# Kernel optimization log

Measured on AMD Instinct MI355X. Metric: run time of the kernel, lower is better.

## Reference

```python
import jax, jax.numpy as jnp
import numpy as np

B, S, D = 2, 2048, 2048
H, HD = 16, 128
P = 2048  # past (cached) kv length


def setup_inputs() -> dict:
    key = jax.random.key(0)
    ks = jax.random.split(key, 12)
    sw = 1.0 / np.sqrt(D)
    inp = {
        "x": jax.random.normal(ks[0], (B, S, D), jnp.float32),
        "past_k": jax.random.normal(ks[1], (B, H, P, HD), jnp.float32),
        "past_v": jax.random.normal(ks[2], (B, H, P, HD), jnp.float32),
        "Wq": jax.random.normal(ks[3], (D, D), jnp.float32) * sw,
        "bq": jax.random.normal(ks[4], (D,), jnp.float32) * 0.01,
        "Wk": jax.random.normal(ks[5], (D, D), jnp.float32) * sw,
        "bk": jax.random.normal(ks[6], (D,), jnp.float32) * 0.01,
        "Wv": jax.random.normal(ks[7], (D, D), jnp.float32) * sw,
        "bv": jax.random.normal(ks[8], (D,), jnp.float32) * 0.01,
        "Wo": jax.random.normal(ks[9], (D, D), jnp.float32) * sw,
        "bo": jax.random.normal(ks[10], (D,), jnp.float32) * 0.01,
    }
    return inp


def _heads(t):
    # [B, S, D] -> [B, H, S, HD]
    return t.reshape(B, -1, H, HD).transpose(0, 2, 1, 3)


def reference(x, past_k, past_v, Wq, bq, Wk, bk, Wv, bv, Wo, bo):
    # QKV projections (separate weights, _qkv_same_embed_dim=False path)
    q = _heads(x @ Wq.T + bq)          # [B,H,S,HD]
    k_new = _heads(x @ Wk.T + bk)      # [B,H,S,HD]
    v_new = _heads(x @ Wv.T + bv)

    # KV cache append
    k_cached = jnp.concatenate([past_k, k_new], axis=2)  # [B,H,P+S,HD]
    v_cached = jnp.concatenate([past_v, v_new], axis=2)
    cached_len = P + S

    # Manual attention path (query_seq_len != cached_seq_len)
    scale = 1.0 / np.sqrt(HD)
    scores = jnp.einsum('bhqd,bhkd->bhqk', q, k_cached) * scale  # [B,H,S,P+S]
    q_pos = jnp.arange(cached_len - S, cached_len)[:, None]
    k_pos = jnp.arange(cached_len)[None, :]
    mask = q_pos >= k_pos  # offset causal mask [S, P+S]
    scores = jnp.where(mask, scores, -jnp.inf)
    attn = jax.nn.softmax(scores, axis=-1)
    out = jnp.einsum('bhqk,bhkd->bhqd', attn, v_cached)  # [B,H,S,HD]

    out = out.transpose(0, 2, 1, 3).reshape(B, S, D)
    return out @ Wo.T + bo
```

## Files before the change

### kernel.cpp

```cpp
#include <hip/hip_runtime.h>

typedef unsigned short u16;
typedef __attribute__((ext_vector_type(4))) float f32x4;
typedef __attribute__((ext_vector_type(8))) short s16x8;

#define CEXP 0.12751742929f

static __device__ __forceinline__ u16 f2bf(float x) {
  unsigned u = __float_as_uint(x);
  u = u + 0x7fffu + ((u >> 16) & 1u);
  return (u16)(u >> 16);
}
static __device__ __forceinline__ unsigned pack2bf(float a, float b) {
  return (unsigned)f2bf(a) | ((unsigned)f2bf(b) << 16);
}
static __device__ __forceinline__ f32x4 fzero() { f32x4 z; z[0]=0.f; z[1]=0.f; z[2]=0.f; z[3]=0.f; return z; }
static __device__ __forceinline__ f32x4 mfma16(s16x8 a, s16x8 b, f32x4 c) {
  return __builtin_amdgcn_mfma_f32_16x16x32_bf16(a, b, c, 0, 0, 0);
}
static __device__ __forceinline__ void gld16(const void* g, void* l) {
  __builtin_amdgcn_global_load_lds((const __attribute__((address_space(1))) void*)g,
                                   (__attribute__((address_space(3))) void*)l, 16, 0, 0);
}

__global__ void cvt_kernel(const float* __restrict__ s, u16* __restrict__ d, int n4, int lg) {
  int stride = gridDim.x * blockDim.x;
  for (int i4 = blockIdx.x * blockDim.x + threadIdx.x; i4 < n4; i4 += stride) {
    int i = i4 * 4;
    float4 v = *reinterpret_cast<const float4*>(s + i);
    size_t di = (size_t)i + ((size_t)(i >> lg) << lg);
    ushort4 o;
    o.x = f2bf(v.x); o.y = f2bf(v.y); o.z = f2bf(v.z); o.w = f2bf(v.w);
    *reinterpret_cast<ushort4*>(d + di) = o;
  }
}

__global__ void transpose_past_v(const float* __restrict__ src, u16* __restrict__ dst) {
  __shared__ u16 tile[64 * 138];
  int bh = blockIdx.y, pt = blockIdx.x;
  const float* s = src + ((size_t)bh * 2048 + (size_t)pt * 64) * 128;
  int t = threadIdx.x;
#pragma unroll
  for (int it = 0; it < 8; ++it) {
    int idx = it * 1024 + t * 4;
    int row = idx >> 7, col = idx & 127;
    float4 v = *reinterpret_cast<const float4*>(s + idx);
    u16* d = &tile[row * 138 + col];
    d[0] = f2bf(v.x); d[1] = f2bf(v.y); d[2] = f2bf(v.z); d[3] = f2bf(v.w);
  }
  __syncthreads();
  size_t dbase = (size_t)bh * 128 * 4096 + (size_t)pt * 64;
#pragma unroll
  for (int it = 0; it < 32; ++it) {
    int o = it * 256 + t;
    int dd = o >> 6, pos = o & 63;
    dst[dbase + (size_t)dd * 4096 + pos] = tile[pos * 138 + dd];
  }
}

__global__ void transpose_new_v(const u16* __restrict__ src, u16* __restrict__ dst) {
  __shared__ u16 tile[64 * 138];
  int bh = blockIdx.y, pt = blockIdx.x;
  const u16* s = src + ((size_t)bh * 2048 + (size_t)pt * 64) * 128;
  int t = threadIdx.x;
#pragma unroll
  for (int it = 0; it < 8; ++it) {
    int idx = it * 1024 + t * 4;
    int row = idx >> 7, col = idx & 127;
    ushort4 v = *reinterpret_cast<const ushort4*>(s + idx);
    u16* d = &tile[row * 138 + col];
    d[0] = v.x; d[1] = v.y; d[2] = v.z; d[3] = v.w;
  }
  __syncthreads();
  size_t dbase = (size_t)bh * 128 * 4096 + 2048 + (size_t)pt * 64;
#pragma unroll
  for (int it = 0; it < 32; ++it) {
    int o = it * 256 + t;
    int dd = o >> 6, pos = o & 63;
    dst[dbase + (size_t)dd * 4096 + pos] = tile[pos * 138 + dd];
  }
}

static __device__ __forceinline__ void gemm_core(const u16* __restrict__ A, const u16* __restrict__ Wn,
                                                 int m0, char* ldsb, f32x4 (&acc)[4][4]) {
  const int tid = threadIdx.x;
  const int w = tid >> 6, lane = tid & 63, g = lane >> 4, ln = lane & 15;
#pragma unroll
  for (int mi = 0; mi < 4; ++mi)
#pragma unroll
    for (int ni = 0; ni < 4; ++ni) acc[mi][ni] = fzero();

  auto stage = [&](int buf, int k0) {
#pragma unroll
    for (int i = 0; i < 2; ++i) {
      int c = w * 2 + i;
      int p = c * 1024 + lane * 16;
      int row = p >> 6;
      int colb = (p & 63) ^ ((row & 3) << 4);
      const u16* sa = A + (size_t)(m0 + row) * 2048 + k0 + (colb >> 1);
      const u16* sw = Wn + (size_t)row * 2048 + k0 + (colb >> 1);
      char* da = ldsb + buf * 16384 + c * 1024;
      gld16(sa, da);
      gld16(sw, da + 8192);
    }
  };
  stage(0, 0);
  __syncthreads();
  const int wr = w >> 1, wc = w & 1;
  for (int kt = 0; kt < 64; ++kt) {
    int cur = kt & 1;
    if (kt < 63) stage(cur ^ 1, (kt + 1) * 32);
    const char* bp = ldsb + cur * 16384;
    s16x8 af[4], bw[4];
#pragma unroll
    for (int mi = 0; mi < 4; ++mi) {
      int row = wr * 64 + mi * 16 + ln;
      int lin = row * 64 + g * 16;
      af[mi] = *reinterpret_cast<const s16x8*>(bp + (lin ^ ((row & 3) << 4)));
    }
#pragma unroll
    for (int ni = 0; ni < 4; ++ni) {
      int row = wc * 64 + ni * 16 + ln;
      int lin = row * 64 + g * 16;
      bw[ni] = *reinterpret_cast<const s16x8*>(bp + 8192 + (lin ^ ((row & 3) << 4)));
    }
#pragma unroll
    for (int mi = 0; mi < 4; ++mi)
#pragma unroll
      for (int ni = 0; ni < 4; ++ni)
        acc[mi][ni] = mfma16(af[mi], bw[ni], acc[mi][ni]);
    __syncthreads();
  }
}

__global__ __launch_bounds__(256, 3) void qkv_gemm(const u16* __restrict__ xb,
    const u16* __restrict__ wq, const u16* __restrict__ wk, const u16* __restrict__ wv,
    const float* __restrict__ bq, const float* __restrict__ bk, const float* __restrict__ bv,
    u16* __restrict__ outq, u16* __restrict__ kc, u16* __restrict__ outv) {
  __shared__ char ldsb[32768];
  int m0 = blockIdx.x * 128;
  int ny = blockIdx.y;
  int wsel = ny >> 4, n0 = (ny & 15) * 128;
  const u16* W; const float* bias; u16* dst; int lrow, off;
  if (wsel == 0)      { W = wq; bias = bq; dst = outq; lrow = 2048; off = 0; }
  else if (wsel == 1) { W = wk; bias = bk; dst = kc;   lrow = 4096; off = 2048; }
  else                { W = wv; bias = bv; dst = outv; lrow = 2048; off = 0; }
  f32x4 acc[4][4];
  gemm_core(xb, W + (size_t)n0 * 2048, m0, ldsb, acc);
  const int tid = threadIdx.x, w = tid >> 6, lane = tid & 63, g = lane >> 4, ln = lane & 15;
  const int wr = w >> 1, wc = w & 1;
#pragma unroll
  for (int ni = 0; ni < 4; ++ni) {
    int j = n0 + wc * 64 + ni * 16 + ln;
    float bcol = bias[j];
    int h = j >> 7, hd = j & 127;
#pragma unroll
    for (int mi = 0; mi < 4; ++mi) {
#pragma unroll
      for (int r = 0; r < 4; ++r) {
        int rowg = m0 + wr * 64 + mi * 16 + g * 4 + r;
        int b = rowg >> 11, s = rowg & 2047;
        float val = acc[mi][ni][r] + bcol;
        dst[((size_t)(b * 16 + h) * lrow + off + s) * 128 + hd] = f2bf(val);
      }
    }
  }
}

__global__ __launch_bounds__(256, 3) void proj_gemm(const u16* __restrict__ ao, const u16* __restrict__ wo,
    const float* __restrict__ bo, float* __restrict__ out) {
  __shared__ char ldsb[32768];
  int m0 = blockIdx.x * 128, n0 = blockIdx.y * 128;
  f32x4 acc[4][4];
  gemm_core(ao, wo + (size_t)n0 * 2048, m0, ldsb, acc);
  const int tid = threadIdx.x, w = tid >> 6, lane = tid & 63, g = lane >> 4, ln = lane & 15;
  const int wr = w >> 1, wc = w & 1;
#pragma unroll
  for (int ni = 0; ni < 4; ++ni) {
    int j = n0 + wc * 64 + ni * 16 + ln;
    float bcol = bo[j];
#pragma unroll
    for (int mi = 0; mi < 4; ++mi) {
#pragma unroll
      for (int r = 0; r < 4; ++r) {
        int rowg = m0 + wr * 64 + mi * 16 + g * 4 + r;
        out[(size_t)rowg * 2048 + j] = acc[mi][ni][r] + bcol;
      }
    }
  }
}

__global__ __launch_bounds__(256, 2) void attn_kernel(const u16* __restrict__ Qb,
    const u16* __restrict__ Kc, const u16* __restrict__ Vt, u16* __restrict__ Ao) {
  __shared__ char lds[65536];
  const int tid = threadIdx.x, w = tid >> 6, lane = tid & 63, g = lane >> 4, ln = lane & 15;
  const int bh = blockIdx.y, qbk = blockIdx.x;
  const int b = bh >> 4, h = bh & 15;
  const u16* Qbh = Qb + (size_t)bh * 2048 * 128;
  const u16* Kbh = Kc + (size_t)bh * 4096 * 128;
  const u16* Vbh = Vt + (size_t)bh * 128 * 4096;

  const int qrow0 = qbk * 128 + w * 32;
  s16x8 qf[2][4];
#pragma unroll
  for (int nt = 0; nt < 2; ++nt)
#pragma unroll
    for (int ks = 0; ks < 4; ++ks)
      qf[nt][ks] = *reinterpret_cast<const s16x8*>(Qbh + (size_t)(qrow0 + nt * 16 + ln) * 128 + ks * 32 + g * 8);

  f32x4 o[2][8];
#pragma unroll
  for (int qt = 0; qt < 2; ++qt)
#pragma unroll
    for (int nd = 0; nd < 8; ++nd) o[qt][nd] = fzero();
  float mrun[2] = {-3e38f, -3e38f}, lrun[2] = {0.f, 0.f};

  const int qpmin = 2048 + qrow0;
  const int ntiles = (2048 + qbk * 128 + 128) >> 6;

  auto stage = [&](int buf, int kv0) {
    char* base = lds + buf * 32768;
#pragma unroll
    for (int i = 0; i < 4; ++i) {
      int p = (w * 4 + i) * 1024 + lane * 16;
      int row = p >> 8;
      int colb = (p & 255) ^ ((row & 7) << 4);
      gld16(Kbh + (size_t)(kv0 + row) * 128 + (colb >> 1), base + (w * 4 + i) * 1024);
      int vrow = p >> 7;
      int vcol = (p & 127) ^ ((vrow & 7) << 4);
      gld16(Vbh + (size_t)vrow * 4096 + kv0 + (vcol >> 1), base + 16384 + (w * 4 + i) * 1024);
    }
  };

  stage(0, 0);
  __syncthreads();
  for (int t = 0; t < ntiles; ++t) {
    int cur = t & 1;
    int kv0 = t * 64;
    if (t + 1 < ntiles) stage(cur ^ 1, kv0 + 64);
    const char* Kl = lds + cur * 32768;
    const char* Vl = Kl + 16384;
    bool active = kv0 <= qpmin + 31;
    if (active) {
      f32x4 sf[4][2];
#pragma unroll
      for (int mt = 0; mt < 4; ++mt) { sf[mt][0] = fzero(); sf[mt][1] = fzero(); }
#pragma unroll
      for (int ks = 0; ks < 4; ++ks) {
#pragma unroll
        for (int mt = 0; mt < 4; ++mt) {
          int row = mt * 16 + ln;
          int lin = row * 256 + ks * 64 + g * 16;
          s16x8 a = *reinterpret_cast<const s16x8*>(Kl + (lin ^ ((row & 7) << 4)));
          sf[mt][0] = mfma16(a, qf[0][ks], sf[mt][0]);
          sf[mt][1] = mfma16(a, qf[1][ks], sf[mt][1]);
        }
      }
      if (kv0 + 63 > qpmin) {
#pragma unroll
        for (int mt = 0; mt < 4; ++mt)
#pragma unroll
          for (int nt = 0; nt < 2; ++nt)
#pragma unroll
            for (int r = 0; r < 4; ++r) {
              int kvg = kv0 + mt * 16 + g * 4 + r;
              int qp = 2048 + qrow0 + nt * 16 + ln;
              if (kvg > qp) sf[mt][nt][r] = -3e38f;
            }
      }
      float fac[2];
#pragma unroll
      for (int nt = 0; nt < 2; ++nt) {
        float pm = sf[0][nt][0];
#pragma unroll
        for (int mt = 0; mt < 4; ++mt)
#pragma unroll
          for (int r = 0; r < 4; ++r) pm = fmaxf(pm, sf[mt][nt][r]);
        pm = fmaxf(pm, __shfl_xor(pm, 16));
        pm = fmaxf(pm, __shfl_xor(pm, 32));
        float mnew = (pm > mrun[nt] + 8.f) ? pm : mrun[nt];
        float f = exp2f((mrun[nt] - mnew) * CEXP);
        mrun[nt] = mnew; fac[nt] = f;
        float rs = 0.f;
#pragma unroll
        for (int mt = 0; mt < 4; ++mt)
#pragma unroll
          for (int r = 0; r < 4; ++r) {
            float p = exp2f((sf[mt][nt][r] - mnew) * CEXP);
            sf[mt][nt][r] = p; rs += p;
          }
        rs += __shfl_xor(rs, 16); rs += __shfl_xor(rs, 32);
        lrun[nt] = lrun[nt] * f + rs;
      }
      if (!__all((fac[0] == 1.f) & (fac[1] == 1.f))) {
#pragma unroll
        for (int qt = 0; qt < 2; ++qt) {
          float fr[4];
#pragma unroll
          for (int r = 0; r < 4; ++r) fr[r] = __shfl(fac[qt], g * 4 + r);
#pragma unroll
          for (int nd = 0; nd < 8; ++nd) {
            o[qt][nd][0] *= fr[0]; o[qt][nd][1] *= fr[1];
            o[qt][nd][2] *= fr[2]; o[qt][nd][3] *= fr[3];
          }
        }
      }
      unsigned pk[4][2][2];
#pragma unroll
      for (int mt = 0; mt < 4; ++mt)
#pragma unroll
        for (int nt = 0; nt < 2; ++nt) {
          pk[mt][nt][0] = pack2bf(sf[mt][nt][0], sf[mt][nt][1]);
          pk[mt][nt][1] = pack2bf(sf[mt][nt][2], sf[mt][nt][3]);
        }
#pragma unroll
      for (int c = 0; c < 2; ++c) {
        s16x8 pa[2];
#pragma unroll
        for (int qt = 0; qt < 2; ++qt) {
          union { unsigned u[4]; s16x8 v; } pu;
#pragma unroll
          for (int j2 = 0; j2 < 4; ++j2) {
            int sdx = j2 >> 1, di = j2 & 1;
            int src = ((2 * (g & 1) + sdx) << 4) | ln;
            unsigned u0 = (unsigned)__shfl((int)pk[2 * c + 0][qt][di], src);
            unsigned u1 = (unsigned)__shfl((int)pk[2 * c + 1][qt][di], src);
            pu.u[j2] = (g & 2) ? u1 : u0;
          }
          pa[qt] = pu.v;
        }
#pragma unroll
        for (int nd = 0; nd < 8; ++nd) {
          int drow = nd * 16 + ln;
          int lin = drow * 128 + c * 64 + g * 16;
          s16x8 bv = *reinterpret_cast<const s16x8*>(Vl + (lin ^ ((drow & 7) << 4)));
          o[0][nd] = mfma16(pa[0], bv, o[0][nd]);
          o[1][nd] = mfma16(pa[1], bv, o[1][nd]);
        }
      }
    }
    __syncthreads();
  }

#pragma unroll
  for (int qt = 0; qt < 2; ++qt) {
    float li[4];
#pragma unroll
    for (int r = 0; r < 4; ++r) li[r] = 1.f / __shfl(lrun[qt], g * 4 + r);
#pragma unroll
    for (int nd = 0; nd < 8; ++nd) {
#pragma unroll
      for (int r = 0; r < 4; ++r) {
        int qrow = qrow0 + qt * 16 + g * 4 + r;
        Ao[((size_t)b * 2048 + qrow) * 2048 + h * 128 + nd * 16 + ln] = f2bf(o[qt][nd][r] * li[r]);
      }
    }
  }
}

extern "C" void kernel_launch(void* const* d_in, const int* in_sizes, int n_in,
                              void* d_out, int out_size, void* d_ws, size_t ws_size,
                              hipStream_t stream) {
  const float* x      = (const float*)d_in[0];
  const float* past_k = (const float*)d_in[1];
  const float* past_v = (const float*)d_in[2];
  const float* Wq = (const float*)d_in[3];
  const float* bq = (const float*)d_in[4];
  const float* Wk = (const float*)d_in[5];
  const float* bk = (const float*)d_in[6];
  const float* Wv = (const float*)d_in[7];
  const float* bv = (const float*)d_in[8];
  const float* Wo = (const float*)d_in[9];
  const float* bo = (const float*)d_in[10];
  float* out = (float*)d_out;

  char* ws = (char*)d_ws;
  u16* xb   = (u16*)(ws);
  u16* wqb  = (u16*)(ws + 16777216);
  u16* wkb  = (u16*)(ws + 25165824);
  u16* wvb  = (u16*)(ws + 33554432);
  u16* wob  = (u16*)(ws + 41943040);
  u16* kc   = (u16*)(ws + 50331648);
  u16* qbuf = (u16*)(ws + 83886080);
  u16* vn   = (u16*)(ws + 100663296);
  u16* vt   = (u16*)(ws + 117440512);
  u16* ao   = xb;

  cvt_kernel<<<1024, 256, 0, stream>>>(x, xb, 2097152, 30);
  cvt_kernel<<<1024, 256, 0, stream>>>(Wq, wqb, 1048576, 30);
  cvt_kernel<<<1024, 256, 0, stream>>>(Wk, wkb, 1048576, 30);
  cvt_kernel<<<1024, 256, 0, stream>>>(Wv, wvb, 1048576, 30);
  cvt_kernel<<<1024, 256, 0, stream>>>(Wo, wob, 1048576, 30);
  cvt_kernel<<<1024, 256, 0, stream>>>(past_k, kc, 2097152, 18);
  transpose_past_v<<<dim3(32, 32), 256, 0, stream>>>(past_v, vt);
  qkv_gemm<<<dim3(32, 48), 256, 0, stream>>>(xb, wqb, wkb, wvb, bq, bk, bv, qbuf, kc, vn);
  transpose_new_v<<<dim3(32, 32), 256, 0, stream>>>(vn, vt);
  attn_kernel<<<dim3(16, 32), 256, 0, stream>>>(qbuf, kc, vt, ao);
  proj_gemm<<<dim3(32, 16), 256, 0, stream>>>(ao, wob, bo, out);
}
```

Before: 456.4 us.

## Rewrite attention inner loop with 32x32 MFMA, permlane swaps and staged output

The attention kernel switches from 16x16x32 to 32x32x16 bf16 MFMA tiles, so each wave holds one 32-row query tile and needs fewer LDS fragment loads and cross-lane shuffles. P is converted with v_cvt_pk_bf16_f32 and re-laid out with permlane32_swap instead of many __shfl calls. Barriers become explicit vmcnt/lgkmcnt waits and s_setprio is raised around the MFMA sections. The grid is reordered to pair short and long causal query blocks, and the output goes through LDS so global stores are coalesced. The new fragment layouts and hand-written waits could break correctness if counts or indices are wrong.

```diff
diff --git a/kernel.cpp b/kernel.cpp
--- a/kernel.cpp
+++ b/kernel.cpp
@@ -2,7 +2,9 @@
 
 typedef unsigned short u16;
 typedef __attribute__((ext_vector_type(4))) float f32x4;
+typedef __attribute__((ext_vector_type(16))) float f32x16;
 typedef __attribute__((ext_vector_type(8))) short s16x8;
+typedef __attribute__((ext_vector_type(2))) unsigned int u32x2v;
 
 #define CEXP 0.12751742929f
 
@@ -11,12 +13,20 @@
   u = u + 0x7fffu + ((u >> 16) & 1u);
   return (u16)(u >> 16);
 }
-static __device__ __forceinline__ unsigned pack2bf(float a, float b) {
-  return (unsigned)f2bf(a) | ((unsigned)f2bf(b) << 16);
+static __device__ __forceinline__ unsigned cvtpk(float a, float b) {
+  unsigned r;
+  asm("v_cvt_pk_bf16_f32 %0, %1, %2" : "=v"(r) : "v"(a), "v"(b));
+  return r;
+}
+static __device__ __forceinline__ u32x2v pswap(unsigned a, unsigned b) {
+  return __builtin_amdgcn_permlane32_swap(a, b, false, false);
 }
 static __device__ __forceinline__ f32x4 fzero() { f32x4 z; z[0]=0.f; z[1]=0.f; z[2]=0.f; z[3]=0.f; return z; }
 static __device__ __forceinline__ f32x4 mfma16(s16x8 a, s16x8 b, f32x4 c) {
   return __builtin_amdgcn_mfma_f32_16x16x32_bf16(a, b, c, 0, 0, 0);
+}
+static __device__ __forceinline__ f32x16 mfma32(s16x8 a, s16x8 b, f32x16 c) {
+  return __builtin_amdgcn_mfma_f32_32x32x16_bf16(a, b, c, 0, 0, 0);
 }
 static __device__ __forceinline__ void gld16(const void* g, void* l) {
   __builtin_amdgcn_global_load_lds((const __attribute__((address_space(1))) void*)g,
@@ -193,30 +203,32 @@
 __global__ __launch_bounds__(256, 2) void attn_kernel(const u16* __restrict__ Qb,
     const u16* __restrict__ Kc, const u16* __restrict__ Vt, u16* __restrict__ Ao) {
   __shared__ char lds[65536];
-  const int tid = threadIdx.x, w = tid >> 6, lane = tid & 63, g = lane >> 4, ln = lane & 15;
-  const int bh = blockIdx.y, qbk = blockIdx.x;
+  const int tid = threadIdx.x, w = tid >> 6, lane = tid & 63;
+  const int hi = lane >> 5, l5 = lane & 31;
+  const int bh = blockIdx.x;
+  const int qy = blockIdx.y;
+  const int qbk = (qy & 8) ? (15 - (qy & 7)) : qy;
   const int b = bh >> 4, h = bh & 15;
   const u16* Qbh = Qb + (size_t)bh * 2048 * 128;
   const u16* Kbh = Kc + (size_t)bh * 4096 * 128;
   const u16* Vbh = Vt + (size_t)bh * 128 * 4096;
 
   const int qrow0 = qbk * 128 + w * 32;
-  s16x8 qf[2][4];
-#pragma unroll
-  for (int nt = 0; nt < 2; ++nt)
-#pragma unroll
-    for (int ks = 0; ks < 4; ++ks)
-      qf[nt][ks] = *reinterpret_cast<const s16x8*>(Qbh + (size_t)(qrow0 + nt * 16 + ln) * 128 + ks * 32 + g * 8);
-
-  f32x4 o[2][8];
-#pragma unroll
-  for (int qt = 0; qt < 2; ++qt)
-#pragma unroll
-    for (int nd = 0; nd < 8; ++nd) o[qt][nd] = fzero();
-  float mrun[2] = {-3e38f, -3e38f}, lrun[2] = {0.f, 0.f};
-
+  const int qp = 2048 + qrow0 + l5;
   const int qpmin = 2048 + qrow0;
   const int ntiles = (2048 + qbk * 128 + 128) >> 6;
+
+  s16x8 qf[8];
+#pragma unroll
+  for (int kc = 0; kc < 8; ++kc)
+    qf[kc] = *reinterpret_cast<const s16x8*>(Qbh + (size_t)(qrow0 + l5) * 128 + kc * 16 + hi * 8);
+
+  f32x16 o[4];
+#pragma unroll
+  for (int dt = 0; dt < 4; ++dt)
+#pragma unroll
+    for (int i = 0; i < 16; ++i) o[dt][i] = 0.f;
+  float mrun = -3e38f, lrun = 0.f;
 
   auto stage = [&](int buf, int kv0) {
     char* base = lds + buf * 32768;
@@ -233,128 +245,131 @@
   };
 
   stage(0, 0);
-  __syncthreads();
   for (int t = 0; t < ntiles; ++t) {
-    int cur = t & 1;
-    int kv0 = t * 64;
-    if (t + 1 < ntiles) stage(cur ^ 1, kv0 + 64);
+    const int kv0 = t * 64;
+    const int cur = t & 1;
+    if (t + 1 < ntiles) {
+      stage(cur ^ 1, kv0 + 64);
+      asm volatile("s_waitcnt vmcnt(8)\n\ts_barrier" ::: "memory");
+    } else {
+      asm volatile("s_waitcnt vmcnt(0)\n\ts_barrier" ::: "memory");
+    }
     const char* Kl = lds + cur * 32768;
     const char* Vl = Kl + 16384;
-    bool active = kv0 <= qpmin + 31;
-    if (active) {
-      f32x4 sf[4][2];
-#pragma unroll
-      for (int mt = 0; mt < 4; ++mt) { sf[mt][0] = fzero(); sf[mt][1] = fzero(); }
-#pragma unroll
-      for (int ks = 0; ks < 4; ++ks) {
-#pragma unroll
-        for (int mt = 0; mt < 4; ++mt) {
-          int row = mt * 16 + ln;
-          int lin = row * 256 + ks * 64 + g * 16;
+    if (kv0 <= qpmin + 31) {
+      f32x16 s0, s1;
+#pragma unroll
+      for (int i = 0; i < 16; ++i) { s0[i] = 0.f; s1[i] = 0.f; }
+      __builtin_amdgcn_s_setprio(1);
+#pragma unroll
+      for (int kc = 0; kc < 8; ++kc) {
+        {
+          int row = l5;
+          int lin = row * 256 + kc * 32 + hi * 16;
           s16x8 a = *reinterpret_cast<const s16x8*>(Kl + (lin ^ ((row & 7) << 4)));
-          sf[mt][0] = mfma16(a, qf[0][ks], sf[mt][0]);
-          sf[mt][1] = mfma16(a, qf[1][ks], sf[mt][1]);
+          s0 = mfma32(a, qf[kc], s0);
         }
-      }
+        {
+          int row = 32 + l5;
+          int lin = row * 256 + kc * 32 + hi * 16;
+          s16x8 a = *reinterpret_cast<const s16x8*>(Kl + (lin ^ ((row & 7) << 4)));
+          s1 = mfma32(a, qf[kc], s1);
+        }
+      }
+      __builtin_amdgcn_s_setprio(0);
       if (kv0 + 63 > qpmin) {
 #pragma unroll
-        for (int mt = 0; mt < 4; ++mt)
-#pragma unroll
-          for (int nt = 0; nt < 2; ++nt)
-#pragma unroll
-            for (int r = 0; r < 4; ++r) {
-              int kvg = kv0 + mt * 16 + g * 4 + r;
-              int qp = 2048 + qrow0 + nt * 16 + ln;
-              if (kvg > qp) sf[mt][nt][r] = -3e38f;
-            }
-      }
-      float fac[2];
-#pragma unroll
-      for (int nt = 0; nt < 2; ++nt) {
-        float pm = sf[0][nt][0];
-#pragma unroll
-        for (int mt = 0; mt < 4; ++mt)
-#pragma unroll
-          for (int r = 0; r < 4; ++r) pm = fmaxf(pm, sf[mt][nt][r]);
-        pm = fmaxf(pm, __shfl_xor(pm, 16));
-        pm = fmaxf(pm, __shfl_xor(pm, 32));
-        float mnew = (pm > mrun[nt] + 8.f) ? pm : mrun[nt];
-        float f = exp2f((mrun[nt] - mnew) * CEXP);
-        mrun[nt] = mnew; fac[nt] = f;
-        float rs = 0.f;
-#pragma unroll
-        for (int mt = 0; mt < 4; ++mt)
-#pragma unroll
-          for (int r = 0; r < 4; ++r) {
-            float p = exp2f((sf[mt][nt][r] - mnew) * CEXP);
-            sf[mt][nt][r] = p; rs += p;
-          }
-        rs += __shfl_xor(rs, 16); rs += __shfl_xor(rs, 32);
-        lrun[nt] = lrun[nt] * f + rs;
-      }
-      if (!__all((fac[0] == 1.f) & (fac[1] == 1.f))) {
-#pragma unroll
-        for (int qt = 0; qt < 2; ++qt) {
-          float fr[4];
-#pragma unroll
-          for (int r = 0; r < 4; ++r) fr[r] = __shfl(fac[qt], g * 4 + r);
-#pragma unroll
-          for (int nd = 0; nd < 8; ++nd) {
-            o[qt][nd][0] *= fr[0]; o[qt][nd][1] *= fr[1];
-            o[qt][nd][2] *= fr[2]; o[qt][nd][3] *= fr[3];
-          }
+        for (int i = 0; i < 16; ++i) {
+          int r0 = (i & 3) + 8 * (i >> 2) + 4 * hi;
+          if (kv0 + r0 > qp) s0[i] = -3e38f;
+          if (kv0 + 32 + r0 > qp) s1[i] = -3e38f;
         }
       }
-      unsigned pk[4][2][2];
-#pragma unroll
-      for (int mt = 0; mt < 4; ++mt)
-#pragma unroll
-        for (int nt = 0; nt < 2; ++nt) {
-          pk[mt][nt][0] = pack2bf(sf[mt][nt][0], sf[mt][nt][1]);
-          pk[mt][nt][1] = pack2bf(sf[mt][nt][2], sf[mt][nt][3]);
+      float pm = s0[0];
+#pragma unroll
+      for (int i = 1; i < 16; ++i) pm = fmaxf(pm, s0[i]);
+#pragma unroll
+      for (int i = 0; i < 16; ++i) pm = fmaxf(pm, s1[i]);
+      {
+        u32x2v rr = pswap(__float_as_uint(pm), __float_as_uint(pm));
+        pm = fmaxf(pm, __uint_as_float(hi ? rr[0] : rr[1]));
+      }
+      float mnew = (pm > mrun + 8.f) ? pm : mrun;
+      float fsc = exp2f((mrun - mnew) * CEXP);
+      mrun = mnew;
+      float rs = 0.f;
+#pragma unroll
+      for (int i = 0; i < 16; ++i) { float p = exp2f((s0[i] - mnew) * CEXP); s0[i] = p; rs += p; }
+#pragma unroll
+      for (int i = 0; i < 16; ++i) { float p = exp2f((s1[i] - mnew) * CEXP); s1[i] = p; rs += p; }
+      {
+        u32x2v rr = pswap(__float_as_uint(rs), __float_as_uint(rs));
+        rs += __uint_as_float(hi ? rr[0] : rr[1]);
+      }
+      lrun = lrun * fsc + rs;
+      if (!__all(fsc == 1.f)) {
+#pragma unroll
+        for (int dt = 0; dt < 4; ++dt)
+#pragma unroll
+          for (int i = 0; i < 16; ++i) o[dt][i] *= fsc;
+      }
+      s16x8 pb[4];
+#pragma unroll
+      for (int c2 = 0; c2 < 4; ++c2) {
+        const f32x16& sv = (c2 & 2) ? s1 : s0;
+        const int b0 = (c2 & 1) * 8;
+        unsigned x0 = cvtpk(sv[b0 + 0], sv[b0 + 1]);
+        unsigned x1 = cvtpk(sv[b0 + 2], sv[b0 + 3]);
+        unsigned y0 = cvtpk(sv[b0 + 4], sv[b0 + 5]);
+        unsigned y1 = cvtpk(sv[b0 + 6], sv[b0 + 7]);
+        u32x2v r0 = pswap(x0, y0);
+        u32x2v r1 = pswap(x1, y1);
+        union { unsigned u[4]; s16x8 v; } pu;
+        pu.u[0] = r0[0]; pu.u[1] = r1[0]; pu.u[2] = r0[1]; pu.u[3] = r1[1];
+        pb[c2] = pu.v;
+      }
+      __builtin_amdgcn_s_setprio(1);
+#pragma unroll
+      for (int dt = 0; dt < 4; ++dt) {
+#pragma unroll
+        for (int c2 = 0; c2 < 4; ++c2) {
+          int row = dt * 32 + l5;
+          int lin = row * 128 + c2 * 32 + hi * 16;
+          s16x8 va = *reinterpret_cast<const s16x8*>(Vl + (lin ^ ((row & 7) << 4)));
+          o[dt] = mfma32(va, pb[c2], o[dt]);
         }
-#pragma unroll
-      for (int c = 0; c < 2; ++c) {
-        s16x8 pa[2];
-#pragma unroll
-        for (int qt = 0; qt < 2; ++qt) {
-          union { unsigned u[4]; s16x8 v; } pu;
-#pragma unroll
-          for (int j2 = 0; j2 < 4; ++j2) {
-            int sdx = j2 >> 1, di = j2 & 1;
-            int src = ((2 * (g & 1) + sdx) << 4) | ln;
-            unsigned u0 = (unsigned)__shfl((int)pk[2 * c + 0][qt][di], src);
-            unsigned u1 = (unsigned)__shfl((int)pk[2 * c + 1][qt][di], src);
-            pu.u[j2] = (g & 2) ? u1 : u0;
-          }
-          pa[qt] = pu.v;
-        }
-#pragma unroll
-        for (int nd = 0; nd < 8; ++nd) {
-          int drow = nd * 16 + ln;
-          int lin = drow * 128 + c * 64 + g * 16;
-          s16x8 bv = *reinterpret_cast<const s16x8*>(Vl + (lin ^ ((drow & 7) << 4)));
-          o[0][nd] = mfma16(pa[0], bv, o[0][nd]);
-          o[1][nd] = mfma16(pa[1], bv, o[1][nd]);
-        }
-      }
-    }
-    __syncthreads();
-  }
-
-#pragma unroll
-  for (int qt = 0; qt < 2; ++qt) {
-    float li[4];
-#pragma unroll
-    for (int r = 0; r < 4; ++r) li[r] = 1.f / __shfl(lrun[qt], g * 4 + r);
-#pragma unroll
-    for (int nd = 0; nd < 8; ++nd) {
-#pragma unroll
-      for (int r = 0; r < 4; ++r) {
-        int qrow = qrow0 + qt * 16 + g * 4 + r;
-        Ao[((size_t)b * 2048 + qrow) * 2048 + h * 128 + nd * 16 + ln] = f2bf(o[qt][nd][r] * li[r]);
-      }
-    }
+      }
+      __builtin_amdgcn_s_setprio(0);
+    }
+    asm volatile("s_waitcnt lgkmcnt(0)\n\ts_barrier" ::: "memory");
+  }
+
+  float li = 1.f / lrun;
+#pragma unroll
+  for (int dt = 0; dt < 4; ++dt)
+#pragma unroll
+    for (int i = 0; i < 16; ++i) o[dt][i] *= li;
+  const int qb = w * 32 + l5;
+#pragma unroll
+  for (int dt = 0; dt < 4; ++dt) {
+#pragma unroll
+    for (int rg = 0; rg < 4; ++rg) {
+      int d0 = dt * 32 + rg * 8 + hi * 4;
+      unsigned w0 = cvtpk(o[dt][rg * 4 + 0], o[dt][rg * 4 + 1]);
+      unsigned w1 = cvtpk(o[dt][rg * 4 + 2], o[dt][rg * 4 + 3]);
+      int lin = qb * 256 + d0 * 2;
+      int phys = lin ^ ((qb & 7) << 4);
+      *reinterpret_cast<uint2*>(lds + phys) = make_uint2(w0, w1);
+    }
+  }
+  __syncthreads();
+  const int qr = tid >> 4, c16 = tid & 15;
+#pragma unroll
+  for (int it = 0; it < 8; ++it) {
+    int q = qr + it * 16;
+    int phys = (q * 256 + c16 * 16) ^ ((q & 7) << 4);
+    s16x8 v = *reinterpret_cast<const s16x8*>(lds + phys);
+    *reinterpret_cast<s16x8*>(Ao + ((size_t)(b * 2048 + qbk * 128 + q)) * 2048 + h * 128 + c16 * 8) = v;
   }
 }
 
@@ -395,6 +410,6 @@
   transpose_past_v<<<dim3(32, 32), 256, 0, stream>>>(past_v, vt);
   qkv_gemm<<<dim3(32, 48), 256, 0, stream>>>(xb, wqb, wkb, wvb, bq, bk, bv, qbuf, kc, vn);
   transpose_new_v<<<dim3(32, 32), 256, 0, stream>>>(vn, vt);
-  attn_kernel<<<dim3(16, 32), 256, 0, stream>>>(qbuf, kc, vt, ao);
+  attn_kernel<<<dim3(32, 16), 256, 0, stream>>>(qbuf, kc, vt, ao);
   proj_gemm<<<dim3(32, 16), 256, 0, stream>>>(ao, wob, bo, out);
 }
```

Result: faster. 390.5 us (-14.4%).
